# Performance work log

Measured on AMD Instinct MI355X. Metric: run time of the kernel, lower is better.

The kernel has to match this reference:

```python
import jax, jax.numpy as jnp
import numpy as np

NEG_SLOPE = 0.2

def _segment_softmax(logits, seg, num_segments):
    m = jax.ops.segment_max(logits, seg, num_segments=num_segments)
    m = jnp.where(jnp.isfinite(m), m, 0.0)
    e = jnp.exp(logits - m[seg])
    s = jax.ops.segment_sum(e, seg, num_segments=num_segments)
    return e / (s[seg] + 1e-16)

def _gat_conv(x, src, dst, W, att_src, att_dst, b):
    # PyG GATConv, heads=1, concat=True, add_self_loops=True
    N = x.shape[0]
    h = x @ W                                   # [N, C]
    a_src = h @ att_src                         # [N]
    a_dst = h @ att_dst                         # [N]
    loop = jnp.arange(N, dtype=src.dtype)
    s = jnp.concatenate([src, loop])            # add self-loops
    d = jnp.concatenate([dst, loop])
    logits = jax.nn.leaky_relu(a_src[s] + a_dst[d], NEG_SLOPE)  # [E+N]
    w = _segment_softmax(logits, d, N)
    out = jax.ops.segment_sum(h[s] * w[:, None], d, num_segments=N)
    return out + b

def _sage_conv(x, src, dst, W_l, W_r, b):
    # PyG SAGEConv, aggr='mean', root_weight=True, normalize=False
    N = x.shape[0]
    agg = jax.ops.segment_sum(x[src], dst, num_segments=N)      # [N, C]
    deg = jax.ops.segment_sum(jnp.ones_like(src, dtype=x.dtype), dst, num_segments=N)
    mean = agg / jnp.maximum(deg, 1.0)[:, None]
    return mean @ W_l + x @ W_r + b

def setup_inputs() -> dict:
    key = jax.random.key(0)
    ks = jax.random.split(key, 12)
    N, E, EL, F_IN, D = 100000, 1000000, 200000, 11, 64
    glorot = lambda k, sh: jax.random.uniform(k, sh, jnp.float32, -1.0, 1.0) * np.sqrt(6.0 / (sh[0] + sh[-1]))
    return {
        "x": jax.random.normal(ks[0], (N, F_IN), jnp.float32),
        "edge_index": jax.random.randint(ks[1], (2, E), 0, N, jnp.int64),
        "edge_label_index": jax.random.randint(ks[2], (2, EL), 0, N, jnp.int64),
        "W_gat": glorot(ks[3], (F_IN, D)),
        "att_src": glorot(ks[4], (D,)),
        "att_dst": glorot(ks[5], (D,)),
        "b_gat": jnp.zeros((D,), jnp.float32),
        "W1_l": glorot(ks[6], (D, D)),
        "W1_r": glorot(ks[7], (D, D)),
        "b1": jnp.zeros((D,), jnp.float32),
        "W2_l": glorot(ks[8], (D, D)),
        "W2_r": glorot(ks[9], (D, D)),
        "b2": jnp.zeros((D,), jnp.float32),
        "alpha": jnp.full((4,), 1.0 / 4.0, jnp.float32),  # num_layers + 1
    }

def reference(x, edge_index, edge_label_index, W_gat, att_src, att_dst, b_gat,
              W1_l, W1_r, b1, W2_l, W2_r, b2, alpha):
    src, dst = edge_index[0], edge_index[1]
    weights = jax.nn.softmax(alpha)
    # Faithful to original get_embedding (note: weights[1] is skipped, as in source)
    h = _gat_conv(x, src, dst, W_gat, att_src, att_dst, b_gat)
    out = h * weights[0]
    h = _sage_conv(h, src, dst, W1_l, W1_r, b1)
    out = out + h * weights[2]
    h = _sage_conv(h, src, dst, W2_l, W2_r, b2)
    out = out + h * weights[3]
    # link prediction: gather + elementwise dot
    return (out[edge_label_index[0]] * out[edge_label_index[1]]).sum(-1)
```

## Files before the change

kernel.cpp:

```cpp
#include <hip/hip_runtime.h>
#include <math.h>
#include <float.h>

#define NEG_SLOPE 0.2f
#define NCHUNK 128

typedef _Float16 half8 __attribute__((ext_vector_type(8)));
typedef float f32x4  __attribute__((ext_vector_type(4)));

__global__ __launch_bounds__(256) void gat_input_kernel(
    const float* __restrict__ x, const float* __restrict__ Wg,
    const float* __restrict__ att_src, const float* __restrict__ att_dst,
    _Float16* __restrict__ Hf, float* __restrict__ a_src, float* __restrict__ a_dst, int N,
    const float* __restrict__ W1l, const float* __restrict__ W1r,
    const float* __restrict__ W2l, const float* __restrict__ W2r,
    _Float16* __restrict__ W1hi, _Float16* __restrict__ W1lo,
    _Float16* __restrict__ W2hi, _Float16* __restrict__ W2lo,
    const float* __restrict__ alpha, float* __restrict__ wsm,
    _Float16* __restrict__ HG, _Float16* __restrict__ H1)
{
    if (blockIdx.x < 8) {
        if (blockIdx.x == 0 && threadIdx.x == 0) {
            float m = alpha[0];
            for (int i = 1; i < 4; i++) m = fmaxf(m, alpha[i]);
            float e[4], s = 0.f;
            for (int i = 0; i < 4; i++) { e[i] = expf(alpha[i] - m); s += e[i]; }
            for (int i = 0; i < 4; i++) wsm[i] = e[i] / s;
        }
        int which = blockIdx.x >> 2;
        const float* Wl = which ? W2l : W1l;
        const float* Wr = which ? W2r : W1r;
        _Float16* Whi = which ? W2hi : W1hi;
        _Float16* Wlo = which ? W2lo : W1lo;
        int idx = (blockIdx.x & 3) * 256 + threadIdx.x;
        int kc = idx >> 8, rem = idx & 255;
        int t = rem >> 6, ln = rem & 63;
        int quad = ln >> 4, col16 = ln & 15;
        int c = t * 16 + col16;
        #pragma unroll
        for (int j = 0; j < 8; j++) {
            int k = kc * 32 + quad * 8 + j;
            float w = (k < 64) ? Wl[k * 64 + c] : Wr[(k - 64) * 64 + c];
            _Float16 hi = (_Float16)w;
            _Float16 lo = (_Float16)(w - (float)hi);
            Whi[(size_t)idx * 8 + j] = hi;
            Wlo[(size_t)idx * 8 + j] = lo;
        }
    } else if (blockIdx.x == 8) {
        if (threadIdx.x < 64) Hf[(size_t)N * 64 + threadIdx.x] = (_Float16)0.f;
        else if (threadIdx.x < 128) HG[(size_t)N * 64 + (threadIdx.x - 64)] = (_Float16)0.f;
        else if (threadIdx.x < 192) H1[(size_t)N * 64 + (threadIdx.x - 128)] = (_Float16)0.f;
        else if (threadIdx.x == 192) a_src[N] = -1e30f;
    }
    __shared__ float Wl[11 * 64];
    int tid = threadIdx.x;
    for (int i = tid; i < 11 * 64; i += 256) Wl[i] = Wg[i];
    __syncthreads();
    int lane = tid & 63;
    int n = blockIdx.x * 4 + (tid >> 6);
    if (n >= N) return;
    float xv = (lane < 11) ? x[n * 11 + lane] : 0.f;
    float acc = 0.f;
    #pragma unroll
    for (int k = 0; k < 11; k++) acc += __shfl(xv, k, 64) * Wl[k * 64 + lane];
    Hf[(size_t)n * 64 + lane] = (_Float16)acc;
    float ps = acc * att_src[lane];
    float pd = acc * att_dst[lane];
    for (int off = 32; off; off >>= 1) {
        ps += __shfl_down(ps, off, 64);
        pd += __shfl_down(pd, off, 64);
    }
    if (lane == 0) { a_src[n] = ps; a_dst[n] = pd; }
}


__global__ __launch_bounds__(1024) void edge_hist_kernel(
    const int* __restrict__ dst, int* __restrict__ hist, int E, int NBK)
{
    __shared__ int c[1024];
    int t = threadIdx.x;
    c[t] = 0;
    __syncthreads();
    int chunk = (E + NCHUNK - 1) / NCHUNK;
    int lo = blockIdx.x * chunk;
    int hi = lo + chunk; if (hi > E) hi = E;
    for (int i = lo + t; i < hi; i += 1024)
        atomicAdd(&c[dst[i] >> 7], 1);
    __syncthreads();
    if (t < NBK) hist[t * NCHUNK + blockIdx.x] = c[t];
}

__global__ __launch_bounds__(1024) void edge_scatter_kernel(
    const int* __restrict__ src, const int* __restrict__ dst,
    const int* __restrict__ rstart, unsigned* __restrict__ ebuf, int E, int NBK)
{
    __shared__ int cur[1024];
    int t = threadIdx.x;
    if (t < NBK) cur[t] = rstart[t * NCHUNK + blockIdx.x];
    __syncthreads();
    int chunk = (E + NCHUNK - 1) / NCHUNK;
    int lo = blockIdx.x * chunk;
    int hi = lo + chunk; if (hi > E) hi = E;
    for (int i = lo + t; i < hi; i += 1024) {
        int d = dst[i];
        int p = atomicAdd(&cur[d >> 7], 1);
        ebuf[p] = ((unsigned)src[i] << 7) | (unsigned)(d & 127);
    }
}

__global__ __launch_bounds__(256) void scan_reduce_kernel(
    const int* __restrict__ v, int* __restrict__ bsum, int M)
{
    __shared__ int s[256];
    int t = threadIdx.x;
    int base = blockIdx.x * 1024 + t * 4;
    int sum = 0;
    #pragma unroll
    for (int j = 0; j < 4; j++) { int idx = base + j; if (idx < M) sum += v[idx]; }
    s[t] = sum; __syncthreads();
    for (int off = 128; off; off >>= 1) {
        if (t < off) s[t] += s[t + off];
        __syncthreads();
    }
    if (t == 0) bsum[blockIdx.x] = s[0];
}

__global__ __launch_bounds__(256) void scan_apply_kernel(
    const int* __restrict__ v, const int* __restrict__ bsum,
    int* __restrict__ out, int M, int NB)
{
    __shared__ int s[256];
    int t = threadIdx.x;
    int bv = (t < NB) ? bsum[t] : 0;
    s[t] = bv; __syncthreads();
    for (int off = 1; off < 256; off <<= 1) {
        int xx = (t >= off) ? s[t - off] : 0;
        __syncthreads();
        s[t] += xx;
        __syncthreads();
    }
    int blockoff = (blockIdx.x == 0) ? 0 : s[blockIdx.x - 1];
    __syncthreads();
    int base = blockIdx.x * 1024;
    int vv[4]; int sum = 0;
    #pragma unroll
    for (int j = 0; j < 4; j++) {
        int idx = base + t * 4 + j;
        vv[j] = (idx < M) ? v[idx] : 0;
        sum += vv[j];
    }
    s[t] = sum; __syncthreads();
    for (int off = 1; off < 256; off <<= 1) {
        int xx = (t >= off) ? s[t - off] : 0;
        __syncthreads();
        s[t] += xx;
        __syncthreads();
    }
    int ex = s[t] - sum + blockoff;
    #pragma unroll
    for (int j = 0; j < 4; j++) {
        int idx = base + t * 4 + j;
        if (idx < M) out[idx] = ex;
        ex += vv[j];
    }
}

__global__ __launch_bounds__(256) void bucket_build_kernel(
    const unsigned* __restrict__ ebuf, const int* __restrict__ rstart,
    int* __restrict__ cnt, int* __restrict__ rowstart,
    int* __restrict__ csr, int E, int N, int NBK)
{
    __shared__ int c[128];
    __shared__ int rs[128];
    __shared__ int cur[128];
    int b = blockIdx.x, t = threadIdx.x;
    if (t < 128) { c[t] = 0; cur[t] = 0; }
    __syncthreads();
    int beg = rstart[b * NCHUNK];
    int end = (b == NBK - 1) ? E : rstart[(b + 1) * NCHUNK];
    int n = end - beg;
    int pbeg = beg + 384 * b;
    for (int j = t; j < n; j += 256)
        atomicAdd(&c[ebuf[beg + j] & 127u], 1);
    __syncthreads();
    int myc = (t < 128) ? c[t] : 0;
    int mypc = (myc + 3) & ~3;
    if (t < 128) rs[t] = mypc;
    __syncthreads();
    for (int off = 1; off < 128; off <<= 1) {
        int v = (t < 128 && t >= off) ? rs[t - off] : 0;
        __syncthreads();
        if (t < 128) rs[t] += v;
        __syncthreads();
    }
    int ex = (t < 128) ? (rs[t] - mypc) : 0;
    __syncthreads();
    if (t < 128) rs[t] = ex;
    int base = b << 7;
    if (t < 128 && base + t < N) {
        cnt[base + t] = myc;
        rowstart[base + t] = pbeg + ex;
    }
    __syncthreads();
    for (int j = t; j < n; j += 256) {
        unsigned e = ebuf[beg + j];
        int d = (int)(e & 127u);
        int p = atomicAdd(&cur[d], 1);
        csr[pbeg + rs[d] + p] = (int)(e >> 7);
    }
    __syncthreads();
    if (t < 128) {
        for (int k = myc; k < mypc; k++) csr[pbeg + rs[t] + k] = N;
    }
}

__global__ __launch_bounds__(256) void gat_gather_kernel(
    const _Float16* __restrict__ Hf, const float* __restrict__ a_src,
    const float* __restrict__ a_dst, const float* __restrict__ bg,
    const int* __restrict__ rowstart, const int* __restrict__ cnt,
    const int* __restrict__ csr, const float* __restrict__ wsm,
    _Float16* __restrict__ HG, _Float16* __restrict__ outD, int N)
{
    const half8* __restrict__ H8 = (const half8*)Hf;
    int tid = threadIdx.x;
    int lane = tid & 63;
    int g = lane >> 3, sub = lane & 7;
    int gl = g << 3;
    int d = blockIdx.x * 32 + (tid >> 3);
    if (d >= N) return;
    float ad = a_dst[d];
    int beg = rowstart[d], deg = cnt[d];
    int degp = (deg + 3) & ~3;
    float a0 = a_src[d] + ad;
    float lg0 = a0 > 0.f ? a0 : NEG_SLOPE * a0;
    float w_self = expf(lg0);
    half8 hself = H8[(size_t)d * 8 + sub];
    float acc[8];
    #pragma unroll
    for (int c = 0; c < 8; c++) acc[c] = w_self * (float)hself[c];
    float l_lane = 0.f;
    for (int base = 0; base < degp; base += 8) {
        int nvc = degp - base; if (nvc > 8) nvc = 8;
        int sid = (sub < nvc) ? csr[beg + base + sub] : N;
        float aa = a_src[sid] + ad;
        float lgt = aa > 0.f ? aa : NEG_SLOPE * aa;
        float w = expf(lgt);
        l_lane += w;
        int ib[8]; float wb[8];
        #pragma unroll
        for (int j = 0; j < 8; j++) {
            ib[j] = __shfl(sid, gl + j, 64);
            wb[j] = __shfl(w, gl + j, 64);
        }
        half8 v[8];
        #pragma unroll
        for (int j = 0; j < 8; j++) v[j] = H8[(size_t)ib[j] * 8 + sub];
        #pragma unroll
        for (int j = 0; j < 8; j++) {
            #pragma unroll
            for (int c = 0; c < 8; c++) acc[c] += wb[j] * (float)v[j][c];
        }
    }
    #pragma unroll
    for (int off = 1; off < 8; off <<= 1) l_lane += __shfl_xor(l_lane, off, 64);
    float l = l_lane + w_self;
    float inv = 1.0f / (l + 1e-16f);
    float w0s = wsm[0];
    size_t idx = (size_t)d * 8 + sub;
    half8 hg, od;
    #pragma unroll
    for (int c = 0; c < 8; c++) {
        float o = acc[c] * inv + bg[sub * 8 + c];
        hg[c] = (_Float16)o;
        od[c] = (_Float16)(w0s * o);
    }
    ((half8*)HG)[idx] = hg;
    ((half8*)outD)[idx] = od;
}

__global__ __launch_bounds__(256) void sage_fused_kernel(
    const _Float16* __restrict__ Hin,
    const _Float16* __restrict__ Whi, const _Float16* __restrict__ Wlo,
    const float* __restrict__ bvec,
    const int* __restrict__ rowstart, const int* __restrict__ cnt,
    const int* __restrict__ csr, const float* __restrict__ wsm, int widx,
    _Float16* __restrict__ hout, _Float16* __restrict__ outD, int N)
{
    __shared__ __align__(16) char smem[64 * 68 * 4];
    float* Ot = (float*)smem;
    const half8* __restrict__ H8 = (const half8*)Hin;
    int tid = threadIdx.x;
    int lane = tid & 63;
    int nodeBase = blockIdx.x * 64;
    int sub = tid & 7;
    int g = lane >> 3;
    int gl = g << 3;

    #pragma unroll
    for (int pass = 0; pass < 2; pass++) {
        int dloc = pass * 32 + (tid >> 3);
        int d = nodeBase + dloc;
        float acc[8];
        #pragma unroll
        for (int c = 0; c < 8; c++) acc[c] = 0.f;
        half8 hself;
        #pragma unroll
        for (int c = 0; c < 8; c++) hself[c] = (_Float16)0.f;
        float invd = 0.f;
        if (d < N) {
            int beg = rowstart[d], deg = cnt[d];
            int degp = (deg + 3) & ~3;
            for (int base2 = 0; base2 < degp; base2 += 8) {
                int nvc = degp - base2; if (nvc > 8) nvc = 8;
                int sid = (sub < nvc) ? csr[beg + base2 + sub] : N;
                int ib[8];
                #pragma unroll
                for (int j = 0; j < 8; j++) ib[j] = __shfl(sid, gl + j, 64);
                half8 v[8];
                #pragma unroll
                for (int j = 0; j < 8; j++) v[j] = H8[(size_t)ib[j] * 8 + sub];
                #pragma unroll
                for (int j = 0; j < 8; j++) {
                    #pragma unroll
                    for (int c = 0; c < 8; c++) acc[c] += (float)v[j][c];
                }
            }
            invd = 1.0f / fmaxf((float)deg, 1.0f);
            hself = H8[(size_t)d * 8 + sub];
        }
        half8 ah;
        #pragma unroll
        for (int c = 0; c < 8; c++) ah[c] = (_Float16)(acc[c] * invd);
        int rbase = dloc * 256;
        int swz = (dloc & 7) << 4;
        *(half8*)(smem + ((rbase + sub * 16) ^ swz)) = ah;
        *(half8*)(smem + ((rbase + 128 + sub * 16) ^ swz)) = hself;
    }
    __syncthreads();

    int quad = lane >> 4, col16 = lane & 15;
    int wave = tid >> 6;
    int row = wave * 16 + col16;
    int rswz = (row & 7) << 4;
    f32x4 accq[4];
    #pragma unroll
    for (int t = 0; t < 4; t++) accq[t] = (f32x4){0.f, 0.f, 0.f, 0.f};
    #pragma unroll
    for (int kc = 0; kc < 4; kc++) {
        half8 a = *(const half8*)(smem + ((row * 256 + kc * 64 + quad * 16) ^ rswz));
        #pragma unroll
        for (int t = 0; t < 4; t++) {
            size_t off = (size_t)((kc * 4 + t) * 64 + lane) * 8;
            half8 bhi = *(const half8*)(Whi + off);
            half8 blo = *(const half8*)(Wlo + off);
            accq[t] = __builtin_amdgcn_mfma_f32_16x16x32_f16(a, bhi, accq[t], 0, 0, 0);
            accq[t] = __builtin_amdgcn_mfma_f32_16x16x32_f16(a, blo, accq[t], 0, 0, 0);
        }
    }
    __syncthreads();
    #pragma unroll
    for (int t = 0; t < 4; t++) {
        #pragma unroll
        for (int r = 0; r < 4; r++) {
            Ot[(wave * 16 + quad * 4 + r) * 68 + t * 16 + col16] = accq[t][r];
        }
    }
    __syncthreads();

    float w = wsm[widx];
    #pragma unroll
    for (int pass = 0; pass < 2; pass++) {
        int dloc = pass * 32 + (tid >> 3);
        int d = nodeBase + dloc;
        if (d >= N) continue;
        size_t idx = (size_t)d * 8 + sub;
        float4 o0 = *(float4*)&Ot[dloc * 68 + sub * 8];
        float4 o1 = *(float4*)&Ot[dloc * 68 + sub * 8 + 4];
        float4 b0 = *(const float4*)&bvec[sub * 8];
        float4 b1 = *(const float4*)&bvec[sub * 8 + 4];
        float o[8] = {o0.x + b0.x, o0.y + b0.y, o0.z + b0.z, o0.w + b0.w,
                      o1.x + b1.x, o1.y + b1.y, o1.z + b1.z, o1.w + b1.w};
        half8 od = ((half8*)outD)[idx];
        half8 ho;
        #pragma unroll
        for (int c = 0; c < 8; c++) {
            ho[c] = (_Float16)o[c];
            od[c] = (_Float16)((float)od[c] + w * o[c]);
        }
        if (hout) ((half8*)hout)[idx] = ho;
        ((half8*)outD)[idx] = od;
    }
}

__global__ __launch_bounds__(256) void link_pred_kernel(
    const int* __restrict__ eli, const _Float16* __restrict__ outf,
    float* __restrict__ out, int EL)
{
    const half8* __restrict__ o8 = (const half8*)outf;
    int e = blockIdx.x * 32 + (threadIdx.x >> 3);
    int sub = threadIdx.x & 7;
    if (e >= EL) return;
    int a = eli[e], b = eli[EL + e];
    half8 pa = o8[(size_t)a * 8 + sub];
    half8 pb = o8[(size_t)b * 8 + sub];
    float p = 0.f;
    #pragma unroll
    for (int c = 0; c < 8; c++) p += (float)pa[c] * (float)pb[c];
    for (int off = 4; off; off >>= 1) p += __shfl_xor(p, off, 64);
    if (sub == 0) out[e] = p;
}

extern "C" void kernel_launch(void* const* d_in, const int* in_sizes, int n_in,
                              void* d_out, int out_size, void* d_ws, size_t ws_size,
                              hipStream_t stream)
{
    const float* x      = (const float*)d_in[0];
    const int*   ei     = (const int*)d_in[1];
    const int*   eli    = (const int*)d_in[2];
    const float* Wg     = (const float*)d_in[3];
    const float* att_s  = (const float*)d_in[4];
    const float* att_d  = (const float*)d_in[5];
    const float* bg     = (const float*)d_in[6];
    const float* W1l    = (const float*)d_in[7];
    const float* W1r    = (const float*)d_in[8];
    const float* b1     = (const float*)d_in[9];
    const float* W2l    = (const float*)d_in[10];
    const float* W2r    = (const float*)d_in[11];
    const float* b2     = (const float*)d_in[12];
    const float* alpha  = (const float*)d_in[13];

    const int N  = in_sizes[0] / 11;
    const int E  = in_sizes[1] / 2;
    const int EL = in_sizes[2] / 2;
    const int NBK = (N + 127) >> 7;
    const int M   = NBK * NCHUNK;
    const int CSRSZ = E + 384 * NBK;

    const int* src = ei;
    const int* dst = ei + E;

    _Float16* Hf  = (_Float16*)d_ws;
    _Float16* HG  = Hf + (size_t)(N + 1) * 64;
    _Float16* H1  = HG + (size_t)(N + 1) * 64;
    _Float16* oD  = H1 + (size_t)(N + 1) * 64;
    _Float16* wf  = oD + (size_t)N * 64;
    _Float16* W1hi = wf;
    _Float16* W1lo = wf + 8192;
    _Float16* W2hi = wf + 16384;
    _Float16* W2lo = wf + 24576;
    float* wsm     = (float*)(wf + 32768);
    float* a_src   = wsm + 4;
    float* a_dst   = a_src + (N + 1);
    int*   cnt     = (int*)(a_dst + N);
    int*   rowstart= cnt + N;
    int*   hist    = rowstart + M ? rowstart + N : rowstart + N;
    int*   rstart  = hist + M;
    int*   bsum    = rstart + M;
    int*   csr     = bsum + 256;
    unsigned* ebuf = (unsigned*)H1;

    gat_input_kernel<<<(N + 3) / 4, 256, 0, stream>>>(x, Wg, att_s, att_d, Hf, a_src, a_dst, N,
                                                      W1l, W1r, W2l, W2r,
                                                      W1hi, W1lo, W2hi, W2lo, alpha, wsm,
                                                      HG, H1);

    edge_hist_kernel<<<NCHUNK, 1024, 0, stream>>>(dst, hist, E, NBK);
    int NB = (M + 1023) / 1024;
    scan_reduce_kernel<<<NB, 256, 0, stream>>>(hist, bsum, M);
    scan_apply_kernel<<<NB, 256, 0, stream>>>(hist, bsum, rstart, M, NB);
    edge_scatter_kernel<<<NCHUNK, 1024, 0, stream>>>(src, dst, rstart, ebuf, E, NBK);
    bucket_build_kernel<<<NBK, 256, 0, stream>>>(ebuf, rstart, cnt, rowstart, csr, E, N, NBK);

    gat_gather_kernel<<<(N + 31) / 32, 256, 0, stream>>>(Hf, a_src, a_dst, bg,
                                                         rowstart, cnt, csr, wsm, HG, oD, N);

    sage_fused_kernel<<<(N + 63) / 64, 256, 0, stream>>>(HG, W1hi, W1lo, b1,
                                                         rowstart, cnt, csr, wsm, 2, H1, oD, N);

    sage_fused_kernel<<<(N + 63) / 64, 256, 0, stream>>>(H1, W2hi, W2lo, b2,
                                                         rowstart, cnt, csr, wsm, 3, nullptr, oD, N);

    link_pred_kernel<<<(EL + 31) / 32, 256, 0, stream>>>(eli, oD, (float*)d_out, EL);
}
```

Before: 248.1 us.

## Fuse edge histogram into GAT input kernel and unroll gathers by sixteen

```diff
diff --git a/kernel.cpp b/kernel.cpp
--- a/kernel.cpp
+++ b/kernel.cpp
@@ -17,10 +17,15 @@
     _Float16* __restrict__ W1hi, _Float16* __restrict__ W1lo,
     _Float16* __restrict__ W2hi, _Float16* __restrict__ W2lo,
     const float* __restrict__ alpha, float* __restrict__ wsm,
-    _Float16* __restrict__ HG, _Float16* __restrict__ H1)
-{
+    _Float16* __restrict__ HG, _Float16* __restrict__ H1,
+    const int* __restrict__ dstArr, int* __restrict__ hist, int E, int NBK)
+{
+    __shared__ __align__(16) char sm[4096 + 4096];
+    float* Wl = (float*)sm;
+    int tid = threadIdx.x;
+
     if (blockIdx.x < 8) {
-        if (blockIdx.x == 0 && threadIdx.x == 0) {
+        if (blockIdx.x == 0 && tid == 0) {
             float m = alpha[0];
             for (int i = 1; i < 4; i++) m = fmaxf(m, alpha[i]);
             float e[4], s = 0.f;
@@ -28,11 +33,11 @@
             for (int i = 0; i < 4; i++) wsm[i] = e[i] / s;
         }
         int which = blockIdx.x >> 2;
-        const float* Wl = which ? W2l : W1l;
-        const float* Wr = which ? W2r : W1r;
+        const float* Wlp = which ? W2l : W1l;
+        const float* Wrp = which ? W2r : W1r;
         _Float16* Whi = which ? W2hi : W1hi;
         _Float16* Wlo = which ? W2lo : W1lo;
-        int idx = (blockIdx.x & 3) * 256 + threadIdx.x;
+        int idx = (blockIdx.x & 3) * 256 + tid;
         int kc = idx >> 8, rem = idx & 255;
         int t = rem >> 6, ln = rem & 63;
         int quad = ln >> 4, col16 = ln & 15;
@@ -40,54 +45,109 @@
         #pragma unroll
         for (int j = 0; j < 8; j++) {
             int k = kc * 32 + quad * 8 + j;
-            float w = (k < 64) ? Wl[k * 64 + c] : Wr[(k - 64) * 64 + c];
+            float w = (k < 64) ? Wlp[k * 64 + c] : Wrp[(k - 64) * 64 + c];
             _Float16 hi = (_Float16)w;
             _Float16 lo = (_Float16)(w - (float)hi);
             Whi[(size_t)idx * 8 + j] = hi;
             Wlo[(size_t)idx * 8 + j] = lo;
         }
     } else if (blockIdx.x == 8) {
-        if (threadIdx.x < 64) Hf[(size_t)N * 64 + threadIdx.x] = (_Float16)0.f;
-        else if (threadIdx.x < 128) HG[(size_t)N * 64 + (threadIdx.x - 64)] = (_Float16)0.f;
-        else if (threadIdx.x < 192) H1[(size_t)N * 64 + (threadIdx.x - 128)] = (_Float16)0.f;
-        else if (threadIdx.x == 192) a_src[N] = -1e30f;
-    }
-    __shared__ float Wl[11 * 64];
-    int tid = threadIdx.x;
+        if (tid < 64) Hf[(size_t)N * 64 + tid] = (_Float16)0.f;
+        else if (tid < 128) HG[(size_t)N * 64 + (tid - 64)] = (_Float16)0.f;
+        else if (tid < 192) H1[(size_t)N * 64 + (tid - 128)] = (_Float16)0.f;
+        else if (tid == 192) a_src[N] = -1e30f;
+    }
+
     for (int i = tid; i < 11 * 64; i += 256) Wl[i] = Wg[i];
     __syncthreads();
     int lane = tid & 63;
     int n = blockIdx.x * 4 + (tid >> 6);
-    if (n >= N) return;
-    float xv = (lane < 11) ? x[n * 11 + lane] : 0.f;
-    float acc = 0.f;
-    #pragma unroll
-    for (int k = 0; k < 11; k++) acc += __shfl(xv, k, 64) * Wl[k * 64 + lane];
-    Hf[(size_t)n * 64 + lane] = (_Float16)acc;
-    float ps = acc * att_src[lane];
-    float pd = acc * att_dst[lane];
-    for (int off = 32; off; off >>= 1) {
-        ps += __shfl_down(ps, off, 64);
-        pd += __shfl_down(pd, off, 64);
-    }
-    if (lane == 0) { a_src[n] = ps; a_dst[n] = pd; }
-}
-
-
-__global__ __launch_bounds__(1024) void edge_hist_kernel(
-    const int* __restrict__ dst, int* __restrict__ hist, int E, int NBK)
-{
-    __shared__ int c[1024];
+    if (n < N) {
+        float xv = (lane < 11) ? x[n * 11 + lane] : 0.f;
+        float acc = 0.f;
+        #pragma unroll
+        for (int k = 0; k < 11; k++) acc += __shfl(xv, k, 64) * Wl[k * 64 + lane];
+        Hf[(size_t)n * 64 + lane] = (_Float16)acc;
+        float ps = acc * att_src[lane];
+        float pd = acc * att_dst[lane];
+        for (int off = 32; off; off >>= 1) {
+            ps += __shfl_down(ps, off, 64);
+            pd += __shfl_down(pd, off, 64);
+        }
+        if (lane == 0) { a_src[n] = ps; a_dst[n] = pd; }
+    }
+
+    int G = (int)gridDim.x;
+    if ((int)blockIdx.x >= G - NCHUNK) {
+        int chunk = (int)blockIdx.x - (G - NCHUNK);
+        int* c = (int*)(sm + 4096);
+        for (int i = tid; i < 1024; i += 256) c[i] = 0;
+        __syncthreads();
+        int cs = (E + NCHUNK - 1) / NCHUNK;
+        int lo = chunk * cs;
+        int hi2 = lo + cs; if (hi2 > E) hi2 = E;
+        for (int i = lo + tid; i < hi2; i += 256)
+            atomicAdd(&c[dstArr[i] >> 7], 1);
+        __syncthreads();
+        for (int t = tid; t < NBK; t += 256) hist[t * NCHUNK + chunk] = c[t];
+    }
+}
+
+__global__ __launch_bounds__(256) void scan_reduce_kernel(
+    const int* __restrict__ v, int* __restrict__ bsum, int M)
+{
+    __shared__ int s[256];
     int t = threadIdx.x;
-    c[t] = 0;
-    __syncthreads();
-    int chunk = (E + NCHUNK - 1) / NCHUNK;
-    int lo = blockIdx.x * chunk;
-    int hi = lo + chunk; if (hi > E) hi = E;
-    for (int i = lo + t; i < hi; i += 1024)
-        atomicAdd(&c[dst[i] >> 7], 1);
-    __syncthreads();
-    if (t < NBK) hist[t * NCHUNK + blockIdx.x] = c[t];
+    int base = blockIdx.x * 1024 + t * 4;
+    int sum = 0;
+    #pragma unroll
+    for (int j = 0; j < 4; j++) { int idx = base + j; if (idx < M) sum += v[idx]; }
+    s[t] = sum; __syncthreads();
+    for (int off = 128; off; off >>= 1) {
+        if (t < off) s[t] += s[t + off];
+        __syncthreads();
+    }
+    if (t == 0) bsum[blockIdx.x] = s[0];
+}
+
+__global__ __launch_bounds__(256) void scan_apply_kernel(
+    const int* __restrict__ v, const int* __restrict__ bsum,
+    int* __restrict__ out, int M, int NB)
+{
+    __shared__ int s[256];
+    int t = threadIdx.x;
+    int bv = (t < NB) ? bsum[t] : 0;
+    s[t] = bv; __syncthreads();
+    for (int off = 1; off < 256; off <<= 1) {
+        int xx = (t >= off) ? s[t - off] : 0;
+        __syncthreads();
+        s[t] += xx;
+        __syncthreads();
+    }
+    int blockoff = (blockIdx.x == 0) ? 0 : s[blockIdx.x - 1];
+    __syncthreads();
+    int base = blockIdx.x * 1024;
+    int vv[4]; int sum = 0;
+    #pragma unroll
+    for (int j = 0; j < 4; j++) {
+        int idx = base + t * 4 + j;
+        vv[j] = (idx < M) ? v[idx] : 0;
+        sum += vv[j];
+    }
+    s[t] = sum; __syncthreads();
+    for (int off = 1; off < 256; off <<= 1) {
+        int xx = (t >= off) ? s[t - off] : 0;
+        __syncthreads();
+        s[t] += xx;
+        __syncthreads();
+    }
+    int ex = s[t] - sum + blockoff;
+    #pragma unroll
+    for (int j = 0; j < 4; j++) {
+        int idx = base + t * 4 + j;
+        if (idx < M) out[idx] = ex;
+        ex += vv[j];
+    }
 }
 
 __global__ __launch_bounds__(1024) void edge_scatter_kernel(
@@ -105,63 +165,6 @@
         int d = dst[i];
         int p = atomicAdd(&cur[d >> 7], 1);
         ebuf[p] = ((unsigned)src[i] << 7) | (unsigned)(d & 127);
-    }
-}
-
-__global__ __launch_bounds__(256) void scan_reduce_kernel(
-    const int* __restrict__ v, int* __restrict__ bsum, int M)
-{
-    __shared__ int s[256];
-    int t = threadIdx.x;
-    int base = blockIdx.x * 1024 + t * 4;
-    int sum = 0;
-    #pragma unroll
-    for (int j = 0; j < 4; j++) { int idx = base + j; if (idx < M) sum += v[idx]; }
-    s[t] = sum; __syncthreads();
-    for (int off = 128; off; off >>= 1) {
-        if (t < off) s[t] += s[t + off];
-        __syncthreads();
-    }
-    if (t == 0) bsum[blockIdx.x] = s[0];
-}
-
-__global__ __launch_bounds__(256) void scan_apply_kernel(
-    const int* __restrict__ v, const int* __restrict__ bsum,
-    int* __restrict__ out, int M, int NB)
-{
-    __shared__ int s[256];
-    int t = threadIdx.x;
-    int bv = (t < NB) ? bsum[t] : 0;
-    s[t] = bv; __syncthreads();
-    for (int off = 1; off < 256; off <<= 1) {
-        int xx = (t >= off) ? s[t - off] : 0;
-        __syncthreads();
-        s[t] += xx;
-        __syncthreads();
-    }
-    int blockoff = (blockIdx.x == 0) ? 0 : s[blockIdx.x - 1];
-    __syncthreads();
-    int base = blockIdx.x * 1024;
-    int vv[4]; int sum = 0;
-    #pragma unroll
-    for (int j = 0; j < 4; j++) {
-        int idx = base + t * 4 + j;
-        vv[j] = (idx < M) ? v[idx] : 0;
-        sum += vv[j];
-    }
-    s[t] = sum; __syncthreads();
-    for (int off = 1; off < 256; off <<= 1) {
-        int xx = (t >= off) ? s[t - off] : 0;
-        __syncthreads();
-        s[t] += xx;
-        __syncthreads();
-    }
-    int ex = s[t] - sum + blockoff;
-    #pragma unroll
-    for (int j = 0; j < 4; j++) {
-        int idx = base + t * 4 + j;
-        if (idx < M) out[idx] = ex;
-        ex += vv[j];
     }
 }
 
@@ -239,26 +242,49 @@
     #pragma unroll
     for (int c = 0; c < 8; c++) acc[c] = w_self * (float)hself[c];
     float l_lane = 0.f;
-    for (int base = 0; base < degp; base += 8) {
-        int nvc = degp - base; if (nvc > 8) nvc = 8;
-        int sid = (sub < nvc) ? csr[beg + base + sub] : N;
-        float aa = a_src[sid] + ad;
-        float lgt = aa > 0.f ? aa : NEG_SLOPE * aa;
-        float w = expf(lgt);
-        l_lane += w;
-        int ib[8]; float wb[8];
-        #pragma unroll
-        for (int j = 0; j < 8; j++) {
-            ib[j] = __shfl(sid, gl + j, 64);
-            wb[j] = __shfl(w, gl + j, 64);
-        }
-        half8 v[8];
-        #pragma unroll
-        for (int j = 0; j < 8; j++) v[j] = H8[(size_t)ib[j] * 8 + sub];
-        #pragma unroll
-        for (int j = 0; j < 8; j++) {
+    for (int base = 0; base < degp; base += 16) {
+        int sidA = (base + sub < degp) ? csr[beg + base + sub] : N;
+        float aaA = a_src[sidA] + ad;
+        float lgA = aaA > 0.f ? aaA : NEG_SLOPE * aaA;
+        float wA = expf(lgA);
+        l_lane += wA;
+        if (degp - base > 8) {
+            int sidB = (base + 8 + sub < degp) ? csr[beg + base + 8 + sub] : N;
+            float aaB = a_src[sidB] + ad;
+            float lgB = aaB > 0.f ? aaB : NEG_SLOPE * aaB;
+            float wB = expf(lgB);
+            l_lane += wB;
+            int ib[16]; float wb[16];
             #pragma unroll
-            for (int c = 0; c < 8; c++) acc[c] += wb[j] * (float)v[j][c];
+            for (int j = 0; j < 8; j++) {
+                ib[j]     = __shfl(sidA, gl + j, 64);
+                wb[j]     = __shfl(wA,   gl + j, 64);
+                ib[8 + j] = __shfl(sidB, gl + j, 64);
+                wb[8 + j] = __shfl(wB,   gl + j, 64);
+            }
+            half8 v[16];
+            #pragma unroll
+            for (int j = 0; j < 16; j++) v[j] = H8[(size_t)ib[j] * 8 + sub];
+            #pragma unroll
+            for (int j = 0; j < 16; j++) {
+                #pragma unroll
+                for (int c = 0; c < 8; c++) acc[c] += wb[j] * (float)v[j][c];
+            }
+        } else {
+            int ib[8]; float wb[8];
+            #pragma unroll
+            for (int j = 0; j < 8; j++) {
+                ib[j] = __shfl(sidA, gl + j, 64);
+                wb[j] = __shfl(wA,   gl + j, 64);
+            }
+            half8 v[8];
+            #pragma unroll
+            for (int j = 0; j < 8; j++) v[j] = H8[(size_t)ib[j] * 8 + sub];
+            #pragma unroll
+            for (int j = 0; j < 8; j++) {
+                #pragma unroll
+                for (int c = 0; c < 8; c++) acc[c] += wb[j] * (float)v[j][c];
+            }
         }
     }
     #pragma unroll
@@ -310,19 +336,36 @@
         if (d < N) {
             int beg = rowstart[d], deg = cnt[d];
             int degp = (deg + 3) & ~3;
-            for (int base2 = 0; base2 < degp; base2 += 8) {
-                int nvc = degp - base2; if (nvc > 8) nvc = 8;
-                int sid = (sub < nvc) ? csr[beg + base2 + sub] : N;
-                int ib[8];
-                #pragma unroll
-                for (int j = 0; j < 8; j++) ib[j] = __shfl(sid, gl + j, 64);
-                half8 v[8];
-                #pragma unroll
-                for (int j = 0; j < 8; j++) v[j] = H8[(size_t)ib[j] * 8 + sub];
-                #pragma unroll
-                for (int j = 0; j < 8; j++) {
+            for (int base2 = 0; base2 < degp; base2 += 16) {
+                int sidA = (base2 + sub < degp) ? csr[beg + base2 + sub] : N;
+                if (degp - base2 > 8) {
+                    int sidB = (base2 + 8 + sub < degp) ? csr[beg + base2 + 8 + sub] : N;
+                    int ib[16];
                     #pragma unroll
-                    for (int c = 0; c < 8; c++) acc[c] += (float)v[j][c];
+                    for (int j = 0; j < 8; j++) {
+                        ib[j]     = __shfl(sidA, gl + j, 64);
+                        ib[8 + j] = __shfl(sidB, gl + j, 64);
+                    }
+                    half8 v[16];
+                    #pragma unroll
+                    for (int j = 0; j < 16; j++) v[j] = H8[(size_t)ib[j] * 8 + sub];
+                    #pragma unroll
+                    for (int j = 0; j < 16; j++) {
+                        #pragma unroll
+                        for (int c = 0; c < 8; c++) acc[c] += (float)v[j][c];
+                    }
+                } else {
+                    int ib[8];
+                    #pragma unroll
+                    for (int j = 0; j < 8; j++) ib[j] = __shfl(sidA, gl + j, 64);
+                    half8 v[8];
+                    #pragma unroll
+                    for (int j = 0; j < 8; j++) v[j] = H8[(size_t)ib[j] * 8 + sub];
+                    #pragma unroll
+                    for (int j = 0; j < 8; j++) {
+                        #pragma unroll
+                        for (int c = 0; c < 8; c++) acc[c] += (float)v[j][c];
+                    }
                 }
             }
             invd = 1.0f / fmaxf((float)deg, 1.0f);
@@ -347,14 +390,14 @@
     for (int t = 0; t < 4; t++) accq[t] = (f32x4){0.f, 0.f, 0.f, 0.f};
     #pragma unroll
     for (int kc = 0; kc < 4; kc++) {
-        half8 a = *(const half8*)(smem + ((row * 256 + kc * 64 + quad * 16) ^ rswz));
+        half8 av = *(const half8*)(smem + ((row * 256 + kc * 64 + quad * 16) ^ rswz));
         #pragma unroll
         for (int t = 0; t < 4; t++) {
             size_t off = (size_t)((kc * 4 + t) * 64 + lane) * 8;
             half8 bhi = *(const half8*)(Whi + off);
             half8 blo = *(const half8*)(Wlo + off);
-            accq[t] = __builtin_amdgcn_mfma_f32_16x16x32_f16(a, bhi, accq[t], 0, 0, 0);
-            accq[t] = __builtin_amdgcn_mfma_f32_16x16x32_f16(a, blo, accq[t], 0, 0, 0);
+            accq[t] = __builtin_amdgcn_mfma_f32_16x16x32_f16(av, bhi, accq[t], 0, 0, 0);
+            accq[t] = __builtin_amdgcn_mfma_f32_16x16x32_f16(av, blo, accq[t], 0, 0, 0);
         }
     }
     __syncthreads();
@@ -377,9 +420,9 @@
         float4 o0 = *(float4*)&Ot[dloc * 68 + sub * 8];
         float4 o1 = *(float4*)&Ot[dloc * 68 + sub * 8 + 4];
         float4 b0 = *(const float4*)&bvec[sub * 8];
-        float4 b1 = *(const float4*)&bvec[sub * 8 + 4];
+        float4 b1v = *(const float4*)&bvec[sub * 8 + 4];
         float o[8] = {o0.x + b0.x, o0.y + b0.y, o0.z + b0.z, o0.w + b0.w,
-                      o1.x + b1.x, o1.y + b1.y, o1.z + b1.z, o1.w + b1.w};
+                      o1.x + b1v.x, o1.y + b1v.y, o1.z + b1v.z, o1.w + b1v.w};
         half8 od = ((half8*)outD)[idx];
         half8 ho;
         #pragma unroll
@@ -434,6 +477,7 @@
     const int EL = in_sizes[2] / 2;
     const int NBK = (N + 127) >> 7;
     const int M   = NBK * NCHUNK;
+    const int NB  = (M + 1023) / 1024;
     const int CSRSZ = E + 384 * NBK;
 
     const int* src = ei;
@@ -453,32 +497,27 @@
     float* a_dst   = a_src + (N + 1);
     int*   cnt     = (int*)(a_dst + N);
     int*   rowstart= cnt + N;
-    int*   hist    = rowstart + M ? rowstart + N : rowstart + N;
+    int*   hist    = rowstart + N;
     int*   rstart  = hist + M;
     int*   bsum    = rstart + M;
     int*   csr     = bsum + 256;
-    unsigned* ebuf = (unsigned*)H1;
-
-    gat_input_kernel<<<(N + 3) / 4, 256, 0, stream>>>(x, Wg, att_s, att_d, Hf, a_src, a_dst, N,
+    unsigned* ebuf = (unsigned*)(csr + CSRSZ);
+
+    gat_input_kernel<<<(N + 3) / 4, 256, 0, stream>>>(x, Wg, att_s, att_d, Hf,
+                                                      a_src, a_dst, N,
                                                       W1l, W1r, W2l, W2r,
-                                                      W1hi, W1lo, W2hi, W2lo, alpha, wsm,
-                                                      HG, H1);
-
-    edge_hist_kernel<<<NCHUNK, 1024, 0, stream>>>(dst, hist, E, NBK);
-    int NB = (M + 1023) / 1024;
+                                                      W1hi, W1lo, W2hi, W2lo,
+                                                      alpha, wsm, HG, H1,
+                                                      dst, hist, E, NBK);
     scan_reduce_kernel<<<NB, 256, 0, stream>>>(hist, bsum, M);
     scan_apply_kernel<<<NB, 256, 0, stream>>>(hist, bsum, rstart, M, NB);
     edge_scatter_kernel<<<NCHUNK, 1024, 0, stream>>>(src, dst, rstart, ebuf, E, NBK);
     bucket_build_kernel<<<NBK, 256, 0, stream>>>(ebuf, rstart, cnt, rowstart, csr, E, N, NBK);
-
     gat_gather_kernel<<<(N + 31) / 32, 256, 0, stream>>>(Hf, a_src, a_dst, bg,
                                                          rowstart, cnt, csr, wsm, HG, oD, N);
-
     sage_fused_kernel<<<(N + 63) / 64, 256, 0, stream>>>(HG, W1hi, W1lo, b1,
                                                          rowstart, cnt, csr, wsm, 2, H1, oD, N);
-
     sage_fused_kernel<<<(N + 63) / 64, 256, 0, stream>>>(H1, W2hi, W2lo, b2,
                                                          rowstart, cnt, csr, wsm, 3, nullptr, oD, N);
-
     link_pred_kernel<<<(EL + 31) / 32, 256, 0, stream>>>(eli, oD, (float*)d_out, EL);
 }
```

Result: slower. 256.2 us (+3.2%).
